# Optimization experiments

Measured on AMD Instinct MI355X. Metric: run time of the kernel, lower is better.

## Reference

```python
import jax, jax.numpy as jnp
import numpy as np

HIDDEN = 512
HEADS = 8
DHEAD = HIDDEN // HEADS  # 64


def setup_inputs() -> dict:
    key = jax.random.key(0)
    ks = jax.random.split(key, 12)
    B, S = 2, 2048
    inp = {
        "q": jax.random.normal(ks[0], (B, S, HIDDEN), dtype=jnp.float32),
        "k": jax.random.normal(ks[1], (B, S, HIDDEN), dtype=jnp.float32),
        "v": jax.random.normal(ks[2], (B, S, HIDDEN), dtype=jnp.float32),
        "mask": jnp.zeros((B, 1, 1, S), dtype=bool),
    }
    scale = 1.0 / np.sqrt(HIDDEN)
    for i, name in enumerate(["Wq", "Wk", "Wv", "Wm"]):
        inp[name] = jax.random.normal(ks[3 + i], (HIDDEN, HIDDEN), dtype=jnp.float32) * scale
    for i, name in enumerate(["bq", "bk", "bv", "bm"]):
        inp[name] = jax.random.normal(ks[7 + i], (HIDDEN,), dtype=jnp.float32) * 0.01
    return inp


def reference(q, k, v, mask, Wq, Wk, Wv, Wm, bq, bk, bv, bm):
    B = q.shape[0]
    # Linear projections (torch Linear: x @ W.T + b)
    qh = (jnp.einsum("bsd,ed->bse", q, Wq) + bq).reshape(B, HEADS, -1, DHEAD)
    kh = (jnp.einsum("bsd,ed->bse", k, Wk) + bk).reshape(B, HEADS, -1, DHEAD)
    vh = (jnp.einsum("bsd,ed->bse", v, Wv) + bv).reshape(B, HEADS, -1, DHEAD)
    # NOTE: the original module reshapes [B,S,512] -> [B,8,S',64] directly
    # (splitting the sequence dim into heads, not the hidden dim); replicated here.
    s = jnp.einsum("bhqd,bhkd->bhqk", qh, kh) / jnp.sqrt(jnp.float32(DHEAD))
    s = jnp.where(mask, jnp.float32(-1e9), s)
    s = jax.nn.softmax(s, axis=-1)
    # dropout is identity in eval mode
    attn = jnp.einsum("bhqk,bhkd->bhqd", s, vh)  # [B,H,S',64]
    attn = attn.transpose(0, 2, 1, 3).reshape(B, -1, HIDDEN)
    return jnp.einsum("bsd,ed->bse", attn, Wm) + bm
```

## Files before the change

### kernel.cpp

```cpp
#include <hip/hip_runtime.h>
#include <hip/hip_bf16.h>
#include <math.h>

typedef float  f32x4 __attribute__((ext_vector_type(4)));
typedef short  s16x8 __attribute__((ext_vector_type(8)));
typedef short  s16x4 __attribute__((ext_vector_type(4)));
typedef unsigned short u16x4 __attribute__((ext_vector_type(4)));

__device__ inline unsigned short bfc(float f){
  __hip_bfloat16 h = __float2bfloat16(f);
  unsigned short u; __builtin_memcpy(&u, &h, 2); return u;
}

__device__ inline f32x4 mfma16(s16x4 a, s16x4 b, f32x4 c){
#if __has_builtin(__builtin_amdgcn_mfma_f32_16x16x16_bf16)
  return __builtin_amdgcn_mfma_f32_16x16x16_bf16(a, b, c, 0, 0, 0);
#elif __has_builtin(__builtin_amdgcn_mfma_f32_16x16x16bf16_1k)
  return __builtin_amdgcn_mfma_f32_16x16x16bf16_1k(a, b, c, 0, 0, 0);
#else
  asm("v_mfma_f32_16x16x16_bf16 %0, %1, %2, %0" : "+v"(c) : "v"(a), "v"(b));
  return c;
#endif
}

__device__ inline void gl_lds16(const unsigned short* g, unsigned short* l){
  __builtin_amdgcn_global_load_lds(
      (const __attribute__((address_space(1))) unsigned int*)g,
      (__attribute__((address_space(3))) unsigned int*)l, 16, 0, 0);
}

__global__ __launch_bounds__(256) void prep(const float* __restrict__ q, const float* __restrict__ k,
                                            const float* __restrict__ v,
                                            const float* __restrict__ w0, const float* __restrict__ w1,
                                            const float* __restrict__ w2, const float* __restrict__ w3,
                                            const unsigned char* __restrict__ mask,
                                            unsigned short* __restrict__ AP, unsigned short* __restrict__ WP,
                                            float* __restrict__ mf){
  int y = blockIdx.y;
  int t = blockIdx.x * 256 + threadIdx.x;
  if (y < 3){
    const float* src = y==0 ? q : (y==1 ? k : v);
    unsigned short* d = AP + (size_t)y * 2097152;
    int r = t >> 6, g = t & 63;
    const float* sp = src + (size_t)r * 512 + g * 8;
    f32x4 a0 = *(const f32x4*)sp;
    f32x4 a1 = *(const f32x4*)(sp + 4);
    s16x8 o = { (short)bfc(a0.x),(short)bfc(a0.y),(short)bfc(a0.z),(short)bfc(a0.w),
                (short)bfc(a1.x),(short)bfc(a1.y),(short)bfc(a1.z),(short)bfc(a1.w) };
    size_t off = ((size_t)(((r>>4)*16 + (g>>2))*64 + (g&3)*16 + (r&15))) * 8;
    *(s16x8*)(d + off) = o;
  } else if (y < 7){
    if (blockIdx.x < 128){
      int yy = y - 3;
      const float* src = yy==0 ? w0 : yy==1 ? w1 : yy==2 ? w2 : w3;
      int c = t >> 6, g = t & 63;
      const float* sp = src + (size_t)c * 512 + g * 8;
      f32x4 a0 = *(const f32x4*)sp;
      f32x4 a1 = *(const f32x4*)(sp + 4);
      s16x8 o = { (short)bfc(a0.x),(short)bfc(a0.y),(short)bfc(a0.z),(short)bfc(a0.w),
                  (short)bfc(a1.x),(short)bfc(a1.y),(short)bfc(a1.z),(short)bfc(a1.w) };
      size_t off = ((size_t)(((c>>4)*16 + (g>>2))*64 + (g&3)*16 + (c&15))) * 8;
      *(s16x8*)(WP + yy*262144 + off) = o;
    }
  } else if (t < 4096){
    int b = t >> 11, kp = t & 2047;
    int korig = (kp & 255) * 8 + (kp >> 8);
    mf[t] = mask[b*2048 + korig] ? -1.442695e9f : 0.0f;
  }
}

__global__ __launch_bounds__(256) void proj_gemm(const unsigned short* __restrict__ Ap,
    const unsigned short* __restrict__ Wp,
    const float* __restrict__ bq, const float* __restrict__ bk, const float* __restrict__ bv,
    unsigned short* __restrict__ pout, unsigned short* __restrict__ Vtp){
  int z = blockIdx.z;
  const unsigned short* A = Ap + (size_t)z * 2097152;
  const unsigned short* W = Wp + (size_t)z * 262144;
  const float* bias = z==0 ? bq : (z==1 ? bk : bv);

  int w = threadIdx.x >> 6, lane = threadIdx.x & 63;
  int lr = lane & 15, lg = lane >> 4;
  int rt = blockIdx.x * 4 + w;
  int bn = blockIdx.y;

  f32x4 acc[4] = {};
  const unsigned short* Abase = A + ((size_t)rt*8192 + lane*8);
  const unsigned short* Wbase = W + ((size_t)bn*32768 + lane*8);
#pragma unroll 4
  for (int kc = 0; kc < 16; ++kc){
    s16x8 af = *(const s16x8*)(Abase + kc*512);
#pragma unroll
    for (int n = 0; n < 4; ++n){
      s16x8 bf = *(const s16x8*)(Wbase + ((size_t)n*16 + kc)*512);
      acc[n] = __builtin_amdgcn_mfma_f32_16x16x32_bf16(af, bf, acc[n], 0, 0, 0);
    }
  }
  if (z == 0){
    unsigned short* out = pout;
    int orow = rt*16 + lg*4;
#pragma unroll
    for (int n = 0; n < 4; ++n){
      int col = bn*64 + n*16 + lr;
      float bv_ = bias[col];
#pragma unroll
      for (int r = 0; r < 4; ++r)
        out[(size_t)(orow + r)*512 + col] = bfc(acc[n][r] + bv_);
    }
  } else if (z == 1){
    int bh = (rt >> 7) * 8 + ((rt >> 4) & 7);
    unsigned short* kp_ = pout + 2097152 + (size_t)bh*131072;
    int kbase = (rt & 15)*16 + 256*bn;
#pragma unroll
    for (int n = 0; n < 4; ++n){
      int col = bn*64 + n*16 + lr;
      float bv_ = bias[col];
#pragma unroll
      for (int r = 0; r < 4; ++r)
        kp_[(size_t)(kbase + lg*4 + r)*64 + n*16 + lr] = bfc(acc[n][r] + bv_);
    }
  } else {
    int bh = (rt >> 7) * 8 + ((rt >> 4) & 7);
    unsigned short* chunk = Vtp + (size_t)bh*131072 + ((size_t)((rt & 15) + 16*bn))*1024;
#pragma unroll
    for (int n = 0; n < 4; ++n){
      int col = bn*64 + n*16 + lr;
      float bv_ = bias[col];
      u16x4 ov = { bfc(acc[n][0] + bv_), bfc(acc[n][1] + bv_),
                   bfc(acc[n][2] + bv_), bfc(acc[n][3] + bv_) };
      *(u16x4*)(chunk + (n*16 + lr)*16 + lg*4) = ov;
    }
  }
}

__global__ __launch_bounds__(512, 4) void flash(const unsigned short* __restrict__ Pq,
                                             const unsigned short* __restrict__ Kp,
                                             const unsigned short* __restrict__ Vtp,
                                             const float* __restrict__ mf,
                                             unsigned short* __restrict__ aout){
  int qt = blockIdx.x;
  int bh = blockIdx.y;
  int b = bh >> 3, h = bh & 7;
  int w = threadIdx.x >> 6;
  int wq = w & 1, wk = w >> 1;
  int lane = threadIdx.x & 63;
  int lr = lane & 15, lg = lane >> 4;

  const unsigned short* Qh  = Pq + (size_t)(b*2048 + h*256)*512;
  const unsigned short* Kh  = Kp + (size_t)bh*131072 + (size_t)wk*32768;
  const unsigned short* Vq  = Vtp + (size_t)bh*131072 + (size_t)wk*32768;
  const float* mp = mf + b*2048 + wk*512 + lg*4;

  __shared__ char smem[65536];
  unsigned short* ktile = (unsigned short*)smem;
  unsigned short* vtile = (unsigned short*)(smem + 32768);
  float* obuf = (float*)smem;
  float* lbuf = (float*)(smem + 49152);

  int krow_l = lane >> 3;
  int cxor  = (lane & 7) ^ krow_l;
  int kcol_l = cxor * 8;

  int vhalf32 = (cxor >> 2) * 32;
  int vkc = (cxor & 3) * 8;
  const unsigned short* kg0 = Kh + (size_t)(8*(wq*2+0) + krow_l)*64 + kcol_l;
  const unsigned short* kg1 = Kh + (size_t)(8*(wq*2+1) + krow_l)*64 + kcol_l;
  int vd0 = wq*16 + krow_l + vhalf32;
  const unsigned short* vg0 = Vq + (vkc>>4)*1024 + vd0*16 + (vkc & 15);
  const unsigned short* vg1 = vg0 + 128;

  s16x8 qf[2][2];
#pragma unroll
  for (int qq = 0; qq < 2; ++qq){
    int qrow = qt*64 + wq*32 + qq*16 + lr;
    qf[qq][0] = *(const s16x8*)(Qh + (size_t)qrow*64 + lg*8);
    qf[qq][1] = *(const s16x8*)(Qh + (size_t)qrow*64 + 32 + lg*8);
  }

  float l[2] = {0.f, 0.f};
  f32x4 accT[2][4] = {};
  int kswz = (lr & 7) * 16;

#define STAGE(dbuf) { \
    unsigned short* kd = ktile + ((dbuf)*4 + wk)*2048; \
    unsigned short* vd = vtile + ((dbuf)*4 + wk)*2048; \
    gl_lds16(kg0, kd + (wq*2+0)*512); \
    gl_lds16(kg1, kd + (wq*2+1)*512); \
    gl_lds16(vg0, vd + (wq*2+0)*512); \
    gl_lds16(vg1, vd + (wq*2+1)*512); \
    kg0 += 2048; kg1 += 2048; vg0 += 2048; vg1 += 2048; }

  STAGE(0)
  f32x4 cmv0 = *(const f32x4*)(mp);
  f32x4 cmv1 = *(const f32x4*)(mp + 16);
  mp += 32;
  __syncthreads();
  int cur = 0;

  for (int t = 0; t < 16; ++t){
    if (t < 15) STAGE(cur ^ 1)
    f32x4 nmv0, nmv1;
    if (t < 15){
      nmv0 = *(const f32x4*)(mp);
      nmv1 = *(const f32x4*)(mp + 16);
      mp += 32;
    }

    const char* kb = (const char*)(ktile + (cur*4 + wk)*2048);
    const char* vb = (const char*)(vtile + (cur*4 + wk)*2048);

    float s2[2][2][4];
    __builtin_amdgcn_s_setprio(1);
#pragma unroll
    for (int n = 0; n < 2; ++n){
      int krow = n*16 + lr;
      s16x8 kf0 = *(const s16x8*)(kb + krow*128 + ((lg*16) ^ kswz));
      s16x8 kf1 = *(const s16x8*)(kb + krow*128 + ((64 + lg*16) ^ kswz));
      f32x4 mv = n ? cmv1 : cmv0;
#pragma unroll
      for (int qq = 0; qq < 2; ++qq){
        f32x4 a = {};
        a = __builtin_amdgcn_mfma_f32_16x16x32_bf16(kf0, qf[qq][0], a, 0, 0, 0);
        a = __builtin_amdgcn_mfma_f32_16x16x32_bf16(kf1, qf[qq][1], a, 0, 0, 0);
#pragma unroll
        for (int r = 0; r < 4; ++r)
          s2[qq][n][r] = __builtin_fmaf(a[r], 0.18033688f, mv[r]);
      }
    }
    __builtin_amdgcn_s_setprio(0);

    s16x4 pf[2][2];
#pragma unroll
    for (int qq = 0; qq < 2; ++qq){
#pragma unroll
      for (int n = 0; n < 2; ++n){
        float p0 = __builtin_amdgcn_exp2f(s2[qq][n][0]);
        float p1 = __builtin_amdgcn_exp2f(s2[qq][n][1]);
        float p2 = __builtin_amdgcn_exp2f(s2[qq][n][2]);
        float p3 = __builtin_amdgcn_exp2f(s2[qq][n][3]);
        l[qq] += (p0 + p1) + (p2 + p3);
        pf[qq][n] = (s16x4){ (short)bfc(p0), (short)bfc(p1), (short)bfc(p2), (short)bfc(p3) };
      }
    }

    __builtin_amdgcn_s_setprio(1);
#pragma unroll
    for (int n = 0; n < 2; ++n){
#pragma unroll
      for (int nd = 0; nd < 4; ++nd){
        int vrow = (nd & 1)*16 + lr;
        int vchunk = ((nd >> 1)*4 + n*2 + (lg >> 1)) ^ (vrow & 7);
        s16x4 vf = *(const s16x4*)(vb + vrow*128 + vchunk*16 + (lg & 1)*8);
        accT[0][nd] = mfma16(vf, pf[0][n], accT[0][nd]);
        accT[1][nd] = mfma16(vf, pf[1][n], accT[1][nd]);
      }
    }
    __builtin_amdgcn_s_setprio(0);

    cmv0 = nmv0; cmv1 = nmv1;
    __syncthreads();
    cur ^= 1;
  }
#undef STAGE

  float lt[2];
#pragma unroll
  for (int qq = 0; qq < 2; ++qq){
    float x = l[qq] + __shfl_xor(l[qq], 16);
    lt[qq] = x + __shfl_xor(x, 32);
  }

  if (wk != 0){
    int j = wk - 1;
#pragma unroll
    for (int qq = 0; qq < 2; ++qq){
      int reg = j*4 + wq*2 + qq;
      if (lg == 0) lbuf[reg*16 + lr] = lt[qq];
#pragma unroll
      for (int nd = 0; nd < 4; ++nd)
        *(f32x4*)&obuf[((size_t)reg*64 + lane)*16 + nd*4] = accT[qq][nd];
    }
  }
  __syncthreads();
  if (wk == 0){
#pragma unroll
    for (int qq = 0; qq < 2; ++qq){
      float ltot = lt[qq];
#pragma unroll
      for (int j = 0; j < 3; ++j)
        ltot += lbuf[(j*4 + wq*2 + qq)*16 + lr];
      float inv = (ltot > 0.f) ? 1.f / ltot : 0.f;
      int q = qt*64 + wq*32 + qq*16 + lr;
      int rt = (b*2048 + q) >> 4;
#pragma unroll
      for (int nd = 0; nd < 4; ++nd){
        f32x4 o = accT[qq][nd];
#pragma unroll
        for (int j = 0; j < 3; ++j){
          int reg = j*4 + wq*2 + qq;
          f32x4 oj = *(const f32x4*)&obuf[((size_t)reg*64 + lane)*16 + nd*4];
          o += oj;
        }
        int g = h*8 + nd*2 + (lg >> 1);
        u16x4 ov = { bfc(o[0]*inv), bfc(o[1]*inv), bfc(o[2]*inv), bfc(o[3]*inv) };
        unsigned short* dp = aout + ((size_t)((rt*16 + (g>>2))*64 + (g&3)*16 + lr))*8 + (lg&1)*4;
        *(u16x4*)dp = ov;
      }
    }
  }
}

__global__ __launch_bounds__(256) void gemm_out(const unsigned short* __restrict__ Ap,
                                                const unsigned short* __restrict__ Wp,
                                                const float* __restrict__ bias,
                                                float* __restrict__ out){
  int w = threadIdx.x >> 6, lane = threadIdx.x & 63;
  int lr = lane & 15, lg = lane >> 4;
  int rt = blockIdx.x * 4 + w;
  int bn = blockIdx.y;
  f32x4 acc[4] = {};
  const unsigned short* Abase = Ap + ((size_t)rt*8192 + lane*8);
  const unsigned short* Wbase = Wp + ((size_t)bn*32768 + lane*8);
#pragma unroll 4
  for (int kc = 0; kc < 16; ++kc){
    s16x8 af = *(const s16x8*)(Abase + kc*512);
#pragma unroll
    for (int n = 0; n < 4; ++n){
      s16x8 bf = *(const s16x8*)(Wbase + ((size_t)n*16 + kc)*512);
      acc[n] = __builtin_amdgcn_mfma_f32_16x16x32_bf16(af, bf, acc[n], 0, 0, 0);
    }
  }
  int orow = rt*16 + lg*4;
#pragma unroll
  for (int n = 0; n < 4; ++n){
    int col = bn*64 + n*16 + lr;
    float bv_ = bias[col];
#pragma unroll
    for (int r = 0; r < 4; ++r)
      out[(size_t)(orow + r)*512 + col] = acc[n][r] + bv_;
  }
}

extern "C" void kernel_launch(void* const* d_in, const int* in_sizes, int n_in,
                              void* d_out, int out_size, void* d_ws, size_t ws_size,
                              hipStream_t stream) {
  const float* q  = (const float*)d_in[0];
  const float* k  = (const float*)d_in[1];
  const float* v  = (const float*)d_in[2];
  const unsigned char* mask = (const unsigned char*)d_in[3];
  const float* Wq = (const float*)d_in[4];
  const float* Wk = (const float*)d_in[5];
  const float* Wv = (const float*)d_in[6];
  const float* Wm = (const float*)d_in[7];
  const float* bq = (const float*)d_in[8];
  const float* bk = (const float*)d_in[9];
  const float* bv = (const float*)d_in[10];
  const float* bm = (const float*)d_in[11];

  unsigned short* ws = (unsigned short*)d_ws;
  unsigned short* WP   = ws;
  float*          MF   = (float*)(ws + 1048576);
  unsigned short* AP   = ws + 1056768;
  unsigned short* PQ   = ws + 7348224;
  unsigned short* VT   = ws + 13639680;
  unsigned short* AO   = ws + 15736832;

  prep<<<dim3(1024, 8), 256, 0, stream>>>(q, k, v, Wq, Wk, Wv, Wm, mask, AP, WP, MF);
  proj_gemm<<<dim3(64, 8, 3), 256, 0, stream>>>(AP, WP, bq, bk, bv, PQ, VT);
  flash<<<dim3(32, 16), 512, 0, stream>>>(PQ, PQ + 2097152, VT, MF, AO);
  gemm_out<<<dim3(64, 8), 256, 0, stream>>>(AO, WP + 3*262144, bm, (float*)d_out);
}
```

Before: 72.93 us.

## Switch flash loop to triple-buffered 16-key stages with vmcnt waits

Replaces the double-buffered 32-key K/V staging with a three-slot ring of 16-key stages, loaded two tiles ahead. Each iteration waits with s_waitcnt vmcnt(2) plus a single barrier instead of a full __syncthreads after compute, so global-to-LDS copies can overlap more compute. Shared memory shrinks from 64KB to about 49KB, which may let more blocks fit per CU. In exchange, the loop runs twice as many iterations with smaller MFMA batches, reads the mask from global every iteration, and issues prefetches past the last tile.

```diff
diff --git a/kernel.cpp b/kernel.cpp
--- a/kernel.cpp
+++ b/kernel.cpp
@@ -145,28 +145,23 @@
   int lane = threadIdx.x & 63;
   int lr = lane & 15, lg = lane >> 4;
 
-  const unsigned short* Qh  = Pq + (size_t)(b*2048 + h*256)*512;
-  const unsigned short* Kh  = Kp + (size_t)bh*131072 + (size_t)wk*32768;
-  const unsigned short* Vq  = Vtp + (size_t)bh*131072 + (size_t)wk*32768;
+  const unsigned short* Qh = Pq + (size_t)(b*2048 + h*256)*512;
+  const unsigned short* Kh = Kp + (size_t)bh*131072 + (size_t)wk*32768;
+  const unsigned short* Vq = Vtp + (size_t)bh*131072 + (size_t)wk*32768;
   const float* mp = mf + b*2048 + wk*512 + lg*4;
 
-  __shared__ char smem[65536];
+  __shared__ char smem[50176];
   unsigned short* ktile = (unsigned short*)smem;
-  unsigned short* vtile = (unsigned short*)(smem + 32768);
+  unsigned short* vtile = (unsigned short*)(smem + 24576);
   float* obuf = (float*)smem;
   float* lbuf = (float*)(smem + 49152);
 
-  int krow_l = lane >> 3;
-  int cxor  = (lane & 7) ^ krow_l;
-  int kcol_l = cxor * 8;
-
-  int vhalf32 = (cxor >> 2) * 32;
-  int vkc = (cxor & 3) * 8;
-  const unsigned short* kg0 = Kh + (size_t)(8*(wq*2+0) + krow_l)*64 + kcol_l;
-  const unsigned short* kg1 = Kh + (size_t)(8*(wq*2+1) + krow_l)*64 + kcol_l;
-  int vd0 = wq*16 + krow_l + vhalf32;
-  const unsigned short* vg0 = Vq + (vkc>>4)*1024 + vd0*16 + (vkc & 15);
-  const unsigned short* vg1 = vg0 + 128;
+  int row_l = lane >> 3;
+  int cxor  = (lane & 7) ^ row_l;
+
+  unsigned short* kg = const_cast<unsigned short*>(Kh) + (size_t)(8*wq + row_l)*64 + cxor*8;
+  unsigned short* vg = const_cast<unsigned short*>(Vq)
+                       + (size_t)(wq*8 + row_l + 16*(cxor>>1))*16 + (cxor&1)*8;
 
   s16x8 qf[2][2];
 #pragma unroll
@@ -180,85 +175,66 @@
   f32x4 accT[2][4] = {};
   int kswz = (lr & 7) * 16;
 
-#define STAGE(dbuf) { \
-    unsigned short* kd = ktile + ((dbuf)*4 + wk)*2048; \
-    unsigned short* vd = vtile + ((dbuf)*4 + wk)*2048; \
-    gl_lds16(kg0, kd + (wq*2+0)*512); \
-    gl_lds16(kg1, kd + (wq*2+1)*512); \
-    gl_lds16(vg0, vd + (wq*2+0)*512); \
-    gl_lds16(vg1, vd + (wq*2+1)*512); \
-    kg0 += 2048; kg1 += 2048; vg0 += 2048; vg1 += 2048; }
+#define STAGE(sb) { \
+    unsigned short* kd = ktile + ((sb)*4 + wk)*1024; \
+    unsigned short* vd = vtile + ((sb)*4 + wk)*1024; \
+    gl_lds16(kg, kd + wq*512); \
+    gl_lds16(vg, vd + wq*512); \
+    kg += 1024; vg += 1024; }
 
   STAGE(0)
-  f32x4 cmv0 = *(const f32x4*)(mp);
-  f32x4 cmv1 = *(const f32x4*)(mp + 16);
-  mp += 32;
-  __syncthreads();
-  int cur = 0;
-
-  for (int t = 0; t < 16; ++t){
-    if (t < 15) STAGE(cur ^ 1)
-    f32x4 nmv0, nmv1;
-    if (t < 15){
-      nmv0 = *(const f32x4*)(mp);
-      nmv1 = *(const f32x4*)(mp + 16);
-      mp += 32;
-    }
-
-    const char* kb = (const char*)(ktile + (cur*4 + wk)*2048);
-    const char* vb = (const char*)(vtile + (cur*4 + wk)*2048);
-
-    float s2[2][2][4];
+  STAGE(1)
+  int cbuf = 0, sbuf = 2;
+
+  for (int t = 0; t < 32; ++t){
+    asm volatile("s_waitcnt vmcnt(2)" ::: "memory");
+    __builtin_amdgcn_s_barrier();
+    __builtin_amdgcn_sched_barrier(0);
+    STAGE(sbuf)
+
+    const char* kb = (const char*)(ktile + (cbuf*4 + wk)*1024);
+    const char* vb = (const char*)(vtile + (cbuf*4 + wk)*1024);
+
+    s16x8 kf0 = *(const s16x8*)(kb + lr*128 + ((lg*16) ^ kswz));
+    s16x8 kf1 = *(const s16x8*)(kb + lr*128 + ((64 + lg*16) ^ kswz));
+    f32x4 mv = *(const f32x4*)(mp);
+    float s2[2][4];
     __builtin_amdgcn_s_setprio(1);
 #pragma unroll
-    for (int n = 0; n < 2; ++n){
-      int krow = n*16 + lr;
-      s16x8 kf0 = *(const s16x8*)(kb + krow*128 + ((lg*16) ^ kswz));
-      s16x8 kf1 = *(const s16x8*)(kb + krow*128 + ((64 + lg*16) ^ kswz));
-      f32x4 mv = n ? cmv1 : cmv0;
-#pragma unroll
-      for (int qq = 0; qq < 2; ++qq){
-        f32x4 a = {};
-        a = __builtin_amdgcn_mfma_f32_16x16x32_bf16(kf0, qf[qq][0], a, 0, 0, 0);
-        a = __builtin_amdgcn_mfma_f32_16x16x32_bf16(kf1, qf[qq][1], a, 0, 0, 0);
-#pragma unroll
-        for (int r = 0; r < 4; ++r)
-          s2[qq][n][r] = __builtin_fmaf(a[r], 0.18033688f, mv[r]);
-      }
+    for (int qq = 0; qq < 2; ++qq){
+      f32x4 a = {};
+      a = __builtin_amdgcn_mfma_f32_16x16x32_bf16(kf0, qf[qq][0], a, 0, 0, 0);
+      a = __builtin_amdgcn_mfma_f32_16x16x32_bf16(kf1, qf[qq][1], a, 0, 0, 0);
+#pragma unroll
+      for (int r = 0; r < 4; ++r)
+        s2[qq][r] = __builtin_fmaf(a[r], 0.18033688f, mv[r]);
     }
     __builtin_amdgcn_s_setprio(0);
 
-    s16x4 pf[2][2];
+    s16x4 pf[2];
 #pragma unroll
     for (int qq = 0; qq < 2; ++qq){
-#pragma unroll
-      for (int n = 0; n < 2; ++n){
-        float p0 = __builtin_amdgcn_exp2f(s2[qq][n][0]);
-        float p1 = __builtin_amdgcn_exp2f(s2[qq][n][1]);
-        float p2 = __builtin_amdgcn_exp2f(s2[qq][n][2]);
-        float p3 = __builtin_amdgcn_exp2f(s2[qq][n][3]);
-        l[qq] += (p0 + p1) + (p2 + p3);
-        pf[qq][n] = (s16x4){ (short)bfc(p0), (short)bfc(p1), (short)bfc(p2), (short)bfc(p3) };
-      }
+      float p0 = __builtin_amdgcn_exp2f(s2[qq][0]);
+      float p1 = __builtin_amdgcn_exp2f(s2[qq][1]);
+      float p2 = __builtin_amdgcn_exp2f(s2[qq][2]);
+      float p3 = __builtin_amdgcn_exp2f(s2[qq][3]);
+      l[qq] += (p0 + p1) + (p2 + p3);
+      pf[qq] = (s16x4){ (short)bfc(p0), (short)bfc(p1), (short)bfc(p2), (short)bfc(p3) };
     }
 
     __builtin_amdgcn_s_setprio(1);
 #pragma unroll
-    for (int n = 0; n < 2; ++n){
-#pragma unroll
-      for (int nd = 0; nd < 4; ++nd){
-        int vrow = (nd & 1)*16 + lr;
-        int vchunk = ((nd >> 1)*4 + n*2 + (lg >> 1)) ^ (vrow & 7);
-        s16x4 vf = *(const s16x4*)(vb + vrow*128 + vchunk*16 + (lg & 1)*8);
-        accT[0][nd] = mfma16(vf, pf[0][n], accT[0][nd]);
-        accT[1][nd] = mfma16(vf, pf[1][n], accT[1][nd]);
-      }
+    for (int nd = 0; nd < 4; ++nd){
+      int p = (nd*2 + (lg >> 1)) ^ (lr & 7);
+      s16x4 vf = *(const s16x4*)(vb + lr*128 + p*16 + (lg & 1)*8);
+      accT[0][nd] = mfma16(vf, pf[0], accT[0][nd]);
+      accT[1][nd] = mfma16(vf, pf[1], accT[1][nd]);
     }
     __builtin_amdgcn_s_setprio(0);
 
-    cmv0 = nmv0; cmv1 = nmv1;
-    __syncthreads();
-    cur ^= 1;
+    mp += 16;
+    cbuf = (cbuf == 2) ? 0 : cbuf + 1;
+    sbuf = (sbuf == 2) ? 0 : sbuf + 1;
   }
 #undef STAGE
 
@@ -268,6 +244,8 @@
     float x = l[qq] + __shfl_xor(l[qq], 16);
     lt[qq] = x + __shfl_xor(x, 32);
   }
+
+  __syncthreads();
 
   if (wk != 0){
     int j = wk - 1;
```

After: 77.77 us. 6.6% more time.
